# Performance work log

Measured on AMD Instinct MI355X. Metric: run time of the kernel, lower is better.

## Reference

```python
import jax, jax.numpy as jnp
import numpy as np

N = 50000
E = 800000
D_IN = 256
D_H = 256


def setup_inputs() -> dict:
    key = jax.random.key(0)
    ks = jax.random.split(key, 8)
    x = jax.random.normal(ks[0], (N, D_IN), dtype=jnp.float32)
    W1 = jax.random.normal(ks[1], (D_H, D_IN), dtype=jnp.float32) * (1.0 / np.sqrt(D_IN))
    b1 = jnp.zeros((D_H,), dtype=jnp.float32)
    W2 = jax.random.normal(ks[2], (D_H, D_H), dtype=jnp.float32) * (1.0 / np.sqrt(D_H))
    b2 = jnp.zeros((D_H,), dtype=jnp.float32)
    gamma = jnp.ones((D_H,), dtype=jnp.float32)
    beta = jnp.zeros((D_H,), dtype=jnp.float32)
    adj_values = jax.random.uniform(ks[3], (E,), dtype=jnp.float32)
    rows = jax.random.randint(ks[4], (E,), 0, N, dtype=jnp.int64)
    cols = jax.random.randint(ks[5], (E,), 0, N, dtype=jnp.int64)
    adj_indices = jnp.stack([rows, cols], axis=0)
    return {"x": x, "W1": W1, "b1": b1, "W2": W2, "b2": b2,
            "gamma": gamma, "beta": beta, "adj_values": adj_values,
            "adj_indices": adj_indices}


def _spmm(adj_indices, adj_values, h, n):
    # out[i] = sum_j A[i, j] * h[j]; COO row=indices[0], col=indices[1]
    rows, cols = adj_indices[0], adj_indices[1]
    msgs = adj_values[:, None] * h[cols]          # [E, D]
    return jax.ops.segment_sum(msgs, rows, num_segments=n)


def _layernorm(h, gamma, beta, eps=1e-5):
    mu = jnp.mean(h, axis=-1, keepdims=True)
    var = jnp.var(h, axis=-1, keepdims=True)
    return (h - mu) * jax.lax.rsqrt(var + eps) * gamma + beta


def reference(x, W1, b1, W2, b2, gamma, beta, adj_values, adj_indices):
    n = x.shape[0]
    h = x @ W1.T + b1
    h = _spmm(adj_indices, adj_values, h, n)
    h = jax.nn.gelu(h, approximate=False)
    h = h @ W2.T + b2
    h = _spmm(adj_indices, adj_values, h, n)
    h = jax.nn.gelu(h, approximate=False)
    h = _layernorm(h + x[:, :h.shape[1]], gamma, beta)
    return h
```

## Files before the change

### kernel.cpp

```cpp
#include <hip/hip_runtime.h>
#include <math.h>

#define DH 256
#define CAP 64

typedef __bf16 bf16x8 __attribute__((ext_vector_type(8)));
typedef float f32x4 __attribute__((ext_vector_type(4)));

__device__ __forceinline__ float gelu_exact(float v) {
    return 0.5f * v * (1.0f + erff(v * 0.70710678118654752f));
}

__device__ __forceinline__ unsigned short f2bf(float f) {
    union { float f; unsigned int u; } v; v.f = f;
    unsigned int u = v.u;
    unsigned int r = (u + 0x7FFFu + ((u >> 16) & 1u)) >> 16;
    return (unsigned short)r;
}

__device__ __forceinline__ float bf2f(unsigned short u) {
    union { unsigned int u; float f; } v;
    v.u = ((unsigned int)u) << 16;
    return v.f;
}

__device__ __forceinline__ void async_copy16(const void* g, void* l) {
    __builtin_amdgcn_global_load_lds(
        (const __attribute__((address_space(1))) void*)g,
        (__attribute__((address_space(3))) void*)l, 16, 0, 0);
}

__global__ void zero_cnt_kernel(int* __restrict__ cnt, int n) {
    int i = blockIdx.x * blockDim.x + threadIdx.x;
    if (i < n) cnt[i] = 0;
}

__global__ void convert4_kernel(const float* __restrict__ in, unsigned short* __restrict__ out, int n4) {
    int i = blockIdx.x * blockDim.x + threadIdx.x;
    if (i >= n4) return;
    float4 v = *(const float4*)(in + (size_t)i * 4);
    ushort4 o;
    o.x = f2bf(v.x); o.y = f2bf(v.y); o.z = f2bf(v.z); o.w = f2bf(v.w);
    *(ushort4*)(out + (size_t)i * 4) = o;
}

__global__ void bucket_kernel(const int* __restrict__ idx, const float* __restrict__ vals,
                              int* __restrict__ cnt, uint2* __restrict__ cvb, int E) {
    int e = blockIdx.x * blockDim.x + threadIdx.x;
    if (e >= E) return;
    int r = idx[e];
    int c = idx[E + e];
    float v = vals[e];
    int p = atomicAdd(&cnt[r], 1);
    if (p < CAP) {
        uint2 ev; ev.x = (unsigned)c; ev.y = __float_as_uint(v);
        cvb[(size_t)r * CAP + p] = ev;
    }
}

__global__ __launch_bounds__(256) void gemm_mfma_kernel(
        const unsigned short* __restrict__ A, const unsigned short* __restrict__ B,
        const float* __restrict__ bias, unsigned short* __restrict__ C, int M) {
    __shared__ char smem[32768];
    char* sA = smem;
    char* sB = smem + 16384;
    const int tid  = threadIdx.x;
    const int lane = tid & 63;
    const int wid  = tid >> 6;
    const int m0   = blockIdx.x * 128;
    const int n0   = blockIdx.y * 128;
    const int wm   = wid >> 1, wn = wid & 1;
    const int l15  = lane & 15, l4 = lane >> 4;
    const int srow   = tid >> 3;
    const int schunk = tid & 7;

    f32x4 acc[4][4] = {};

    for (int k0 = 0; k0 < 256; k0 += 64) {
        #pragma unroll
        for (int i = 0; i < 4; ++i) {
            int row = i * 32 + srow;
            int sw  = schunk ^ (row & 7);
            int gra = m0 + row; if (gra >= M) gra = M - 1;
            async_copy16(A + (size_t)gra * DH + k0 + sw * 8,
                         sA + ((size_t)(i * 256 + wid * 64)) * 16);
            async_copy16(B + (size_t)(n0 + row) * DH + k0 + sw * 8,
                         sB + ((size_t)(i * 256 + wid * 64)) * 16);
        }
        __syncthreads();

        bf16x8 af[4][2], bfg[4][2];
        #pragma unroll
        for (int f = 0; f < 4; ++f) {
            int ra = wm * 64 + f * 16 + l15;
            int rb = wn * 64 + f * 16 + l15;
            #pragma unroll
            for (int kf = 0; kf < 2; ++kf) {
                int ca = ((kf * 4 + l4) ^ (ra & 7)) * 16;
                int cb = ((kf * 4 + l4) ^ (rb & 7)) * 16;
                af[f][kf]  = *(const bf16x8*)(sA + ra * 128 + ca);
                bfg[f][kf] = *(const bf16x8*)(sB + rb * 128 + cb);
            }
        }
        #pragma unroll
        for (int fm = 0; fm < 4; ++fm)
            #pragma unroll
            for (int fn = 0; fn < 4; ++fn) {
                acc[fm][fn] = __builtin_amdgcn_mfma_f32_16x16x32_bf16(af[fm][0], bfg[fn][0], acc[fm][fn], 0, 0, 0);
                acc[fm][fn] = __builtin_amdgcn_mfma_f32_16x16x32_bf16(af[fm][1], bfg[fn][1], acc[fm][fn], 0, 0, 0);
            }
        __syncthreads();
    }

    #pragma unroll
    for (int fn = 0; fn < 4; ++fn) {
        float bb = bias[n0 + wn * 64 + fn * 16 + l15];
        #pragma unroll
        for (int fm = 0; fm < 4; ++fm) {
            int mrow = m0 + wm * 64 + fm * 16 + l4 * 4;
            unsigned short* cp = C + (size_t)mrow * DH + n0 + wn * 64 + fn * 16 + l15;
            #pragma unroll
            for (int r = 0; r < 4; ++r) {
                if (mrow + r < M) cp[(size_t)r * DH] = f2bf(acc[fm][fn][r] + bb);
            }
        }
    }
}

template<int MODE>
__global__ __launch_bounds__(256) void spmm_kernel(
        const unsigned short* __restrict__ h, const int* __restrict__ cnt,
        const uint2* __restrict__ cvb, const unsigned short* __restrict__ xres,
        const float* __restrict__ gamma, const float* __restrict__ beta,
        void* __restrict__ outp, int n) {
    const int wv = threadIdx.x >> 6;
    const int lane = threadIdx.x & 63;
    const int row = blockIdx.x * 4 + wv;
    if (row >= n) return;
    int deg = cnt[row]; if (deg > CAP) deg = CAP;
    const uint2* cb = cvb + (size_t)row * CAP;

    float ax = 0.f, ay = 0.f, az = 0.f, aw = 0.f;
    int j = 0;
    for (; j + 4 <= deg; j += 4) {
        uint2 e0 = cb[j], e1 = cb[j + 1], e2 = cb[j + 2], e3 = cb[j + 3];
        ushort4 p0 = *(const ushort4*)(h + (size_t)e0.x * DH + lane * 4);
        ushort4 p1 = *(const ushort4*)(h + (size_t)e1.x * DH + lane * 4);
        ushort4 p2 = *(const ushort4*)(h + (size_t)e2.x * DH + lane * 4);
        ushort4 p3 = *(const ushort4*)(h + (size_t)e3.x * DH + lane * 4);
        float v0 = __uint_as_float(e0.y), v1 = __uint_as_float(e1.y);
        float v2 = __uint_as_float(e2.y), v3 = __uint_as_float(e3.y);
        ax += v0 * bf2f(p0.x) + v1 * bf2f(p1.x) + v2 * bf2f(p2.x) + v3 * bf2f(p3.x);
        ay += v0 * bf2f(p0.y) + v1 * bf2f(p1.y) + v2 * bf2f(p2.y) + v3 * bf2f(p3.y);
        az += v0 * bf2f(p0.z) + v1 * bf2f(p1.z) + v2 * bf2f(p2.z) + v3 * bf2f(p3.z);
        aw += v0 * bf2f(p0.w) + v1 * bf2f(p1.w) + v2 * bf2f(p2.w) + v3 * bf2f(p3.w);
    }
    for (; j < deg; ++j) {
        uint2 e0 = cb[j];
        ushort4 p0 = *(const ushort4*)(h + (size_t)e0.x * DH + lane * 4);
        float v0 = __uint_as_float(e0.y);
        ax += v0 * bf2f(p0.x); ay += v0 * bf2f(p0.y);
        az += v0 * bf2f(p0.z); aw += v0 * bf2f(p0.w);
    }

    ax = gelu_exact(ax); ay = gelu_exact(ay); az = gelu_exact(az); aw = gelu_exact(aw);

    if (MODE == 1) {
        ushort4 xr = *(const ushort4*)(xres + (size_t)row * DH + lane * 4);
        ax += bf2f(xr.x); ay += bf2f(xr.y); az += bf2f(xr.z); aw += bf2f(xr.w);
        float s  = ax + ay + az + aw;
        float s2 = ax * ax + ay * ay + az * az + aw * aw;
        #pragma unroll
        for (int off = 32; off > 0; off >>= 1) {
            s  += __shfl_xor(s,  off);
            s2 += __shfl_xor(s2, off);
        }
        float mu  = s * (1.0f / 256.0f);
        float var = s2 * (1.0f / 256.0f) - mu * mu;
        float rs  = rsqrtf(var + 1e-5f);
        float4 g  = *(const float4*)(gamma + lane * 4);
        float4 bt = *(const float4*)(beta + lane * 4);
        float4 o;
        o.x = (ax - mu) * rs * g.x + bt.x;
        o.y = (ay - mu) * rs * g.y + bt.y;
        o.z = (az - mu) * rs * g.z + bt.z;
        o.w = (aw - mu) * rs * g.w + bt.w;
        *(float4*)((float*)outp + (size_t)row * DH + lane * 4) = o;
    } else {
        ushort4 o;
        o.x = f2bf(ax); o.y = f2bf(ay); o.z = f2bf(az); o.w = f2bf(aw);
        *(ushort4*)((unsigned short*)outp + (size_t)row * DH + lane * 4) = o;
    }
}

extern "C" void kernel_launch(void* const* d_in, const int* in_sizes, int n_in,
                              void* d_out, int out_size, void* d_ws, size_t ws_size,
                              hipStream_t stream) {
    const float* x     = (const float*)d_in[0];
    const float* W1    = (const float*)d_in[1];
    const float* b1    = (const float*)d_in[2];
    const float* W2    = (const float*)d_in[3];
    const float* b2    = (const float*)d_in[4];
    const float* gamma = (const float*)d_in[5];
    const float* beta  = (const float*)d_in[6];
    const float* avals = (const float*)d_in[7];
    const int*   aidx  = (const int*)d_in[8];

    const int n = in_sizes[0] / DH;
    const int e = in_sizes[7];
    float* out = (float*)d_out;

    unsigned short* g1b = (unsigned short*)d_out;

    char* ws = (char*)d_ws;
    size_t off = 0;
    unsigned short* xb  = (unsigned short*)(ws + off); off += (size_t)n * DH * 2;
    off = (off + 255) & ~(size_t)255;
    unsigned short* hb  = (unsigned short*)(ws + off); off += (size_t)n * DH * 2;
    off = (off + 255) & ~(size_t)255;
    unsigned short* W1b = (unsigned short*)(ws + off); off += (size_t)DH * DH * 2;
    off = (off + 255) & ~(size_t)255;
    unsigned short* W2b = (unsigned short*)(ws + off); off += (size_t)DH * DH * 2;
    off = (off + 255) & ~(size_t)255;
    int* cnt = (int*)(ws + off);                       off += (size_t)n * sizeof(int);
    off = (off + 255) & ~(size_t)255;
    uint2* cvb = (uint2*)(ws + off);                   off += (size_t)n * CAP * sizeof(uint2);

    const int gemm_gx = (n + 127) / 128;

    convert4_kernel<<<(DH * DH / 4 + 255) / 256, 256, 0, stream>>>(W1, W1b, DH * DH / 4);
    convert4_kernel<<<(DH * DH / 4 + 255) / 256, 256, 0, stream>>>(W2, W2b, DH * DH / 4);
    convert4_kernel<<<((n * DH / 4) + 255) / 256, 256, 0, stream>>>(x, xb, n * DH / 4);
    zero_cnt_kernel<<<(n + 255) / 256, 256, 0, stream>>>(cnt, n);
    bucket_kernel<<<(e + 255) / 256, 256, 0, stream>>>(aidx, avals, cnt, cvb, e);

    gemm_mfma_kernel<<<dim3(gemm_gx, 2), 256, 0, stream>>>(xb, W1b, b1, hb, n);

    spmm_kernel<0><<<(n + 3) / 4, 256, 0, stream>>>(
        hb, cnt, cvb, nullptr, nullptr, nullptr, g1b, n);

    gemm_mfma_kernel<<<dim3(gemm_gx, 2), 256, 0, stream>>>(g1b, W2b, b2, hb, n);

    spmm_kernel<1><<<(n + 3) / 4, 256, 0, stream>>>(
        hb, cnt, cvb, xb, gamma, beta, out, n);
}
```

Baseline: 249.6 us.

## Fuse x bf16 conversion into GEMM, merge prep kernels, widen SpMM lanes

Drops the separate x-to-bf16 conversion pass. The first GEMM now loads fp32 x directly and converts it while staging into LDS, and the residual in the final SpMM reads fp32 x. The weight conversions and count zeroing are merged into one prep kernel, cutting launch count. SpMM now gives each row 32 lanes with 8 bf16 per lane (16-byte gathers), so one block covers 8 rows. The fp32 A path uses synchronous loads instead of async LDS copies and reads x once per column tile, which may slow the first GEMM.

```diff
diff --git a/kernel.cpp b/kernel.cpp
--- a/kernel.cpp
+++ b/kernel.cpp
@@ -6,6 +6,7 @@
 
 typedef __bf16 bf16x8 __attribute__((ext_vector_type(8)));
 typedef float f32x4 __attribute__((ext_vector_type(4)));
+typedef unsigned short us8 __attribute__((ext_vector_type(8)));
 
 __device__ __forceinline__ float gelu_exact(float v) {
     return 0.5f * v * (1.0f + erff(v * 0.70710678118654752f));
@@ -30,18 +31,27 @@
         (__attribute__((address_space(3))) void*)l, 16, 0, 0);
 }
 
-__global__ void zero_cnt_kernel(int* __restrict__ cnt, int n) {
-    int i = blockIdx.x * blockDim.x + threadIdx.x;
-    if (i < n) cnt[i] = 0;
-}
-
-__global__ void convert4_kernel(const float* __restrict__ in, unsigned short* __restrict__ out, int n4) {
-    int i = blockIdx.x * blockDim.x + threadIdx.x;
-    if (i >= n4) return;
-    float4 v = *(const float4*)(in + (size_t)i * 4);
-    ushort4 o;
-    o.x = f2bf(v.x); o.y = f2bf(v.y); o.z = f2bf(v.z); o.w = f2bf(v.w);
-    *(ushort4*)(out + (size_t)i * 4) = o;
+__global__ void prep_kernel(const float* __restrict__ W1, const float* __restrict__ W2,
+                            unsigned short* __restrict__ W1b, unsigned short* __restrict__ W2b,
+                            int* __restrict__ cnt, int n) {
+    const int WV = DH * DH / 4;
+    int gid = blockIdx.x * blockDim.x + threadIdx.x;
+    if (gid < 2 * WV) {
+        const float* src = (gid < WV) ? W1 : W2;
+        unsigned short* dst = (gid < WV) ? W1b : W2b;
+        int i = (gid < WV) ? gid : gid - WV;
+        float4 v = *(const float4*)(src + (size_t)i * 4);
+        ushort4 o;
+        o.x = f2bf(v.x); o.y = f2bf(v.y); o.z = f2bf(v.z); o.w = f2bf(v.w);
+        *(ushort4*)(dst + (size_t)i * 4) = o;
+    } else {
+        int i = (gid - 2 * WV) * 4;
+        if (i < n) {
+            int4 z = {0, 0, 0, 0};
+            if (i + 4 <= n) *(int4*)(cnt + i) = z;
+            else for (int k = i; k < n; ++k) cnt[k] = 0;
+        }
+    }
 }
 
 __global__ void bucket_kernel(const int* __restrict__ idx, const float* __restrict__ vals,
@@ -58,8 +68,9 @@
     }
 }
 
+template<bool AF32>
 __global__ __launch_bounds__(256) void gemm_mfma_kernel(
-        const unsigned short* __restrict__ A, const unsigned short* __restrict__ B,
+        const void* __restrict__ Ap, const unsigned short* __restrict__ B,
         const float* __restrict__ bias, unsigned short* __restrict__ C, int M) {
     __shared__ char smem[32768];
     char* sA = smem;
@@ -82,8 +93,20 @@
             int row = i * 32 + srow;
             int sw  = schunk ^ (row & 7);
             int gra = m0 + row; if (gra >= M) gra = M - 1;
-            async_copy16(A + (size_t)gra * DH + k0 + sw * 8,
-                         sA + ((size_t)(i * 256 + wid * 64)) * 16);
+            if (AF32) {
+                const float* a32 = (const float*)Ap + (size_t)gra * DH + k0 + schunk * 8;
+                float4 lo = *(const float4*)a32;
+                float4 hi = *(const float4*)(a32 + 4);
+                uint4 pk;
+                pk.x = (unsigned)f2bf(lo.x) | ((unsigned)f2bf(lo.y) << 16);
+                pk.y = (unsigned)f2bf(lo.z) | ((unsigned)f2bf(lo.w) << 16);
+                pk.z = (unsigned)f2bf(hi.x) | ((unsigned)f2bf(hi.y) << 16);
+                pk.w = (unsigned)f2bf(hi.z) | ((unsigned)f2bf(hi.w) << 16);
+                *(uint4*)(sA + row * 128 + sw * 16) = pk;
+            } else {
+                async_copy16((const unsigned short*)Ap + (size_t)gra * DH + k0 + sw * 8,
+                             sA + ((size_t)(i * 256 + wid * 64)) * 16);
+            }
             async_copy16(B + (size_t)(n0 + row) * DH + k0 + sw * 8,
                          sB + ((size_t)(i * 256 + wid * 64)) * 16);
         }
@@ -130,66 +153,80 @@
 template<int MODE>
 __global__ __launch_bounds__(256) void spmm_kernel(
         const unsigned short* __restrict__ h, const int* __restrict__ cnt,
-        const uint2* __restrict__ cvb, const unsigned short* __restrict__ xres,
+        const uint2* __restrict__ cvb, const float* __restrict__ xres,
         const float* __restrict__ gamma, const float* __restrict__ beta,
         void* __restrict__ outp, int n) {
-    const int wv = threadIdx.x >> 6;
-    const int lane = threadIdx.x & 63;
-    const int row = blockIdx.x * 4 + wv;
+    const int l32 = threadIdx.x & 31;
+    const int row = blockIdx.x * 8 + (threadIdx.x >> 5);
     if (row >= n) return;
     int deg = cnt[row]; if (deg > CAP) deg = CAP;
     const uint2* cb = cvb + (size_t)row * CAP;
 
-    float ax = 0.f, ay = 0.f, az = 0.f, aw = 0.f;
+    float a[8] = {};
     int j = 0;
     for (; j + 4 <= deg; j += 4) {
         uint2 e0 = cb[j], e1 = cb[j + 1], e2 = cb[j + 2], e3 = cb[j + 3];
-        ushort4 p0 = *(const ushort4*)(h + (size_t)e0.x * DH + lane * 4);
-        ushort4 p1 = *(const ushort4*)(h + (size_t)e1.x * DH + lane * 4);
-        ushort4 p2 = *(const ushort4*)(h + (size_t)e2.x * DH + lane * 4);
-        ushort4 p3 = *(const ushort4*)(h + (size_t)e3.x * DH + lane * 4);
+        us8 p0 = *(const us8*)(h + (size_t)e0.x * DH + l32 * 8);
+        us8 p1 = *(const us8*)(h + (size_t)e1.x * DH + l32 * 8);
+        us8 p2 = *(const us8*)(h + (size_t)e2.x * DH + l32 * 8);
+        us8 p3 = *(const us8*)(h + (size_t)e3.x * DH + l32 * 8);
         float v0 = __uint_as_float(e0.y), v1 = __uint_as_float(e1.y);
         float v2 = __uint_as_float(e2.y), v3 = __uint_as_float(e3.y);
-        ax += v0 * bf2f(p0.x) + v1 * bf2f(p1.x) + v2 * bf2f(p2.x) + v3 * bf2f(p3.x);
-        ay += v0 * bf2f(p0.y) + v1 * bf2f(p1.y) + v2 * bf2f(p2.y) + v3 * bf2f(p3.y);
-        az += v0 * bf2f(p0.z) + v1 * bf2f(p1.z) + v2 * bf2f(p2.z) + v3 * bf2f(p3.z);
-        aw += v0 * bf2f(p0.w) + v1 * bf2f(p1.w) + v2 * bf2f(p2.w) + v3 * bf2f(p3.w);
+        #pragma unroll
+        for (int d = 0; d < 8; ++d)
+            a[d] += v0 * bf2f(p0[d]) + v1 * bf2f(p1[d]) + v2 * bf2f(p2[d]) + v3 * bf2f(p3[d]);
     }
     for (; j < deg; ++j) {
         uint2 e0 = cb[j];
-        ushort4 p0 = *(const ushort4*)(h + (size_t)e0.x * DH + lane * 4);
+        us8 p0 = *(const us8*)(h + (size_t)e0.x * DH + l32 * 8);
         float v0 = __uint_as_float(e0.y);
-        ax += v0 * bf2f(p0.x); ay += v0 * bf2f(p0.y);
-        az += v0 * bf2f(p0.z); aw += v0 * bf2f(p0.w);
-    }
-
-    ax = gelu_exact(ax); ay = gelu_exact(ay); az = gelu_exact(az); aw = gelu_exact(aw);
+        #pragma unroll
+        for (int d = 0; d < 8; ++d) a[d] += v0 * bf2f(p0[d]);
+    }
+
+    #pragma unroll
+    for (int d = 0; d < 8; ++d) a[d] = gelu_exact(a[d]);
 
     if (MODE == 1) {
-        ushort4 xr = *(const ushort4*)(xres + (size_t)row * DH + lane * 4);
-        ax += bf2f(xr.x); ay += bf2f(xr.y); az += bf2f(xr.z); aw += bf2f(xr.w);
-        float s  = ax + ay + az + aw;
-        float s2 = ax * ax + ay * ay + az * az + aw * aw;
-        #pragma unroll
-        for (int off = 32; off > 0; off >>= 1) {
+        const float* xp = xres + (size_t)row * DH + l32 * 8;
+        float4 x0 = *(const float4*)xp;
+        float4 x1 = *(const float4*)(xp + 4);
+        a[0] += x0.x; a[1] += x0.y; a[2] += x0.z; a[3] += x0.w;
+        a[4] += x1.x; a[5] += x1.y; a[6] += x1.z; a[7] += x1.w;
+        float s = 0.f, s2 = 0.f;
+        #pragma unroll
+        for (int d = 0; d < 8; ++d) { s += a[d]; s2 += a[d] * a[d]; }
+        #pragma unroll
+        for (int off = 16; off > 0; off >>= 1) {
             s  += __shfl_xor(s,  off);
             s2 += __shfl_xor(s2, off);
         }
         float mu  = s * (1.0f / 256.0f);
         float var = s2 * (1.0f / 256.0f) - mu * mu;
         float rs  = rsqrtf(var + 1e-5f);
-        float4 g  = *(const float4*)(gamma + lane * 4);
-        float4 bt = *(const float4*)(beta + lane * 4);
-        float4 o;
-        o.x = (ax - mu) * rs * g.x + bt.x;
-        o.y = (ay - mu) * rs * g.y + bt.y;
-        o.z = (az - mu) * rs * g.z + bt.z;
-        o.w = (aw - mu) * rs * g.w + bt.w;
-        *(float4*)((float*)outp + (size_t)row * DH + lane * 4) = o;
+        const float* gp = gamma + l32 * 8;
+        const float* bp = beta + l32 * 8;
+        float4 g0 = *(const float4*)gp, g1 = *(const float4*)(gp + 4);
+        float4 b0 = *(const float4*)bp, b1 = *(const float4*)(bp + 4);
+        float* op = (float*)outp + (size_t)row * DH + l32 * 8;
+        float4 o0, o1;
+        o0.x = (a[0] - mu) * rs * g0.x + b0.x;
+        o0.y = (a[1] - mu) * rs * g0.y + b0.y;
+        o0.z = (a[2] - mu) * rs * g0.z + b0.z;
+        o0.w = (a[3] - mu) * rs * g0.w + b0.w;
+        o1.x = (a[4] - mu) * rs * g1.x + b1.x;
+        o1.y = (a[5] - mu) * rs * g1.y + b1.y;
+        o1.z = (a[6] - mu) * rs * g1.z + b1.z;
+        o1.w = (a[7] - mu) * rs * g1.w + b1.w;
+        *(float4*)op = o0;
+        *(float4*)(op + 4) = o1;
     } else {
-        ushort4 o;
-        o.x = f2bf(ax); o.y = f2bf(ay); o.z = f2bf(az); o.w = f2bf(aw);
-        *(ushort4*)((unsigned short*)outp + (size_t)row * DH + lane * 4) = o;
+        uint4 pk;
+        pk.x = (unsigned)f2bf(a[0]) | ((unsigned)f2bf(a[1]) << 16);
+        pk.y = (unsigned)f2bf(a[2]) | ((unsigned)f2bf(a[3]) << 16);
+        pk.z = (unsigned)f2bf(a[4]) | ((unsigned)f2bf(a[5]) << 16);
+        pk.w = (unsigned)f2bf(a[6]) | ((unsigned)f2bf(a[7]) << 16);
+        *(uint4*)((unsigned short*)outp + (size_t)row * DH + l32 * 8) = pk;
     }
 }
 
@@ -214,8 +251,6 @@
 
     char* ws = (char*)d_ws;
     size_t off = 0;
-    unsigned short* xb  = (unsigned short*)(ws + off); off += (size_t)n * DH * 2;
-    off = (off + 255) & ~(size_t)255;
     unsigned short* hb  = (unsigned short*)(ws + off); off += (size_t)n * DH * 2;
     off = (off + 255) & ~(size_t)255;
     unsigned short* W1b = (unsigned short*)(ws + off); off += (size_t)DH * DH * 2;
@@ -227,20 +262,18 @@
     uint2* cvb = (uint2*)(ws + off);                   off += (size_t)n * CAP * sizeof(uint2);
 
     const int gemm_gx = (n + 127) / 128;
-
-    convert4_kernel<<<(DH * DH / 4 + 255) / 256, 256, 0, stream>>>(W1, W1b, DH * DH / 4);
-    convert4_kernel<<<(DH * DH / 4 + 255) / 256, 256, 0, stream>>>(W2, W2b, DH * DH / 4);
-    convert4_kernel<<<((n * DH / 4) + 255) / 256, 256, 0, stream>>>(x, xb, n * DH / 4);
-    zero_cnt_kernel<<<(n + 255) / 256, 256, 0, stream>>>(cnt, n);
+    const int prep_items = 2 * (DH * DH / 4) + (n + 3) / 4;
+
+    prep_kernel<<<(prep_items + 255) / 256, 256, 0, stream>>>(W1, W2, W1b, W2b, cnt, n);
     bucket_kernel<<<(e + 255) / 256, 256, 0, stream>>>(aidx, avals, cnt, cvb, e);
 
-    gemm_mfma_kernel<<<dim3(gemm_gx, 2), 256, 0, stream>>>(xb, W1b, b1, hb, n);
-
-    spmm_kernel<0><<<(n + 3) / 4, 256, 0, stream>>>(
+    gemm_mfma_kernel<true><<<dim3(gemm_gx, 2), 256, 0, stream>>>(x, W1b, b1, hb, n);
+
+    spmm_kernel<0><<<(n + 7) / 8, 256, 0, stream>>>(
         hb, cnt, cvb, nullptr, nullptr, nullptr, g1b, n);
 
-    gemm_mfma_kernel<<<dim3(gemm_gx, 2), 256, 0, stream>>>(g1b, W2b, b2, hb, n);
-
-    spmm_kernel<1><<<(n + 3) / 4, 256, 0, stream>>>(
-        hb, cnt, cvb, xb, gamma, beta, out, n);
-}
+    gemm_mfma_kernel<false><<<dim3(gemm_gx, 2), 256, 0, stream>>>(g1b, W2b, b2, hb, n);
+
+    spmm_kernel<1><<<(n + 7) / 8, 256, 0, stream>>>(
+        hb, cnt, cvb, x, gamma, beta, out, n);
+}
```

Result: no change. 248.2 us (-0.5%).
